# Kernel tuning notes

Measured on AMD Instinct MI355X. Metric: run time of the kernel, lower is better.

Reference implementation:

```python
import jax, jax.numpy as jnp
import numpy as np


def setup_inputs() -> dict:
    key = jax.random.key(0)
    k1, k2 = jax.random.split(key)
    N, T, D = 65536, 128, 2
    source = jax.random.normal(k1, (N, T, D), dtype=jnp.float32)
    mask = jax.random.randint(k2, (N, T, D), 0, 2).astype(jnp.float32)
    # Fixed (non-trainable) inertia-model matrices, as in the torch module.
    A = jnp.array([[0.0, 0.0, -1.0, 0.0],
                   [0.0, 0.0, 0.0, -1.0],
                   [0.0, 0.0, 0.0, 0.0],
                   [0.0, 0.0, 0.0, 0.0]], dtype=jnp.float32)
    B = jnp.array([[1.0, 0.0, 1.0, 0.0],
                   [0.0, 1.0, 0.0, 1.0]], dtype=jnp.float32)
    C = jnp.array([[0.0, 0.0],
                   [0.0, 0.0],
                   [1.0, 0.0],
                   [0.0, 1.0]], dtype=jnp.float32)
    return {"source": source, "mask": mask, "A": A, "B": B, "C": C,
            "burn_in_steps": 64}


def reference(source, mask, A, B, C, burn_in_steps):
    # use_mask=True variant of the Inertia model.
    N, T, D = source.shape
    state_dim = 4
    burn_in = int(burn_in_steps)

    src_t = jnp.swapaxes(source, 0, 1)  # [T, N, D]
    msk_t = jnp.swapaxes(mask, 0, 1)    # [T, N, D]
    ts = jnp.arange(T)

    s0 = jnp.zeros((N, state_dim), dtype=source.dtype)
    m0 = jnp.zeros((N, D), dtype=source.dtype)
    y0 = jnp.zeros((N, D), dtype=source.dtype)  # never used on first step

    def step(carry, inp):
        s, m, y = carry
        x_t, mask_t, t = inp
        in_burn = (burn_in <= 0) | (t < burn_in)  # scalar bool
        m_prev = m
        m_new = jnp.where(in_burn, mask_t, m)     # mask only advances in burn-in
        s_app = (1.0 - m_prev) * m_new            # [N, 2]
        x = jnp.where(in_burn, x_t, y)
        s_temp = s @ A + x @ B                    # [N, 4]
        s_next = jnp.concatenate(
            [s_temp[:, :2],
             s[:, 2:4] * s_app + s_temp[:, 2:4] * (1.0 - s_app)], axis=1)
        del_x = s_next @ C                        # [N, 2]
        y_new = x + del_x
        return (s_next, m_new, y_new), y_new

    _, pred = jax.lax.scan(step, (s0, m0, y0), (src_t, msk_t, ts))
    return jnp.swapaxes(pred, 0, 1)  # [N, T, D]
```

## Files before the change

### kernel.cpp

```cpp
#include <hip/hip_runtime.h>


__global__ __launch_bounds__(256) void inertia_scan(
    const float* __restrict__ src, const float* __restrict__ msk,
    float* __restrict__ out, int nseq)
{
    const int n = (blockIdx.x * 256 + threadIdx.x) >> 6;
    const int lane = threadIdx.x & 63;
    if (n >= nseq) return;
    const size_t base = (size_t)n * 128;
    const float2* __restrict__ s2 = (const float2*)src + base;
    const float2* __restrict__ m2 = (const float2*)msk + base;
    float2* __restrict__ o2 = (float2*)out + base;

    float2 sv = s2[lane];
    float2 mv = m2[lane];

    float spx = __shfl_up(sv.x, 1, 64);
    float spy = __shfl_up(sv.y, 1, 64);
    float mpx = __shfl_up(mv.x, 1, 64);
    float mpy = __shfl_up(mv.y, 1, 64);
    const bool l0 = (lane == 0);
    spx = l0 ? 0.f : spx;  spy = l0 ? 0.f : spy;
    mpx = l0 ? 0.f : mpx;  mpy = l0 ? 0.f : mpy;

    float A0 = (1.f - mpx) * mv.x;
    float A1 = (1.f - mpy) * mv.y;
    float B0 = (sv.x - spx) * (1.f - A0);
    float B1 = (sv.y - spy) * (1.f - A1);

#pragma unroll
    for (int off = 1; off < 64; off <<= 1) {
        float Ap0 = __shfl_up(A0, off, 64);
        float Bp0 = __shfl_up(B0, off, 64);
        float Ap1 = __shfl_up(A1, off, 64);
        float Bp1 = __shfl_up(B1, off, 64);
        const bool act = (lane >= off);
        Ap0 = act ? Ap0 : 1.f;  Bp0 = act ? Bp0 : 0.f;
        Ap1 = act ? Ap1 : 1.f;  Bp1 = act ? Bp1 : 0.f;
        B0 = fmaf(Bp0, A0, B0);  A0 *= Ap0;
        B1 = fmaf(Bp1, A1, B1);  A1 *= Ap1;
    }

    const float y0 = sv.x + B0;
    const float y1 = sv.y + B1;
    o2[lane] = make_float2(y0, y1);

    const float q63x = __shfl(B0, 63, 64);
    const float q63y = __shfl(B1, 63, 64);
    const float y63x = __shfl(y0, 63, 64);
    const float y63y = __shfl(y1, 63, 64);
    const float tj = (float)(lane + 1);
    o2[64 + lane] = make_float2(fmaf(tj, q63x, y63x), fmaf(tj, q63y, y63y));
}

extern "C" void kernel_launch(void* const* d_in, const int* in_sizes, int n_in,
                              void* d_out, int out_size, void* d_ws, size_t ws_size,
                              hipStream_t stream) {
    const float* src = (const float*)d_in[0];
    const float* msk = (const float*)d_in[1];
    float* out = (float*)d_out;
    const int nseq = in_sizes[0] / 256;
    const int block = 256;
    const int grid = (nseq + 3) / 4;
    inertia_scan<<<grid, block, 0, stream>>>(src, msk, out, nseq);
}
```

Baseline: 159.9 us.

## Replace shuffle-based affine scan with ballot lookup of last reset lane

Because the mask is binary, each recurrence coefficient A is either 0 or 1, and B is zero wherever A is 1. The prefix result is therefore just B at the most recent lane where A is 0. The six-step log-depth shuffle scan is replaced by one ballot per channel, a leading-zero count and a single shuffle, cutting cross-lane traffic and ALU work. This assumes mask values are exactly 0 or 1; non-binary masks would give wrong results.

```diff
diff --git a/kernel.cpp b/kernel.cpp
--- a/kernel.cpp
+++ b/kernel.cpp
@@ -24,30 +24,28 @@
     spx = l0 ? 0.f : spx;  spy = l0 ? 0.f : spy;
     mpx = l0 ? 0.f : mpx;  mpy = l0 ? 0.f : mpy;
 
-    float A0 = (1.f - mpx) * mv.x;
-    float A1 = (1.f - mpy) * mv.y;
-    float B0 = (sv.x - spx) * (1.f - A0);
-    float B1 = (sv.y - spy) * (1.f - A1);
+    const float A0 = (1.f - mpx) * mv.x;
+    const float A1 = (1.f - mpy) * mv.y;
+    const float B0 = (sv.x - spx) * (1.f - A0);
+    const float B1 = (sv.y - spy) * (1.f - A1);
 
-#pragma unroll
-    for (int off = 1; off < 64; off <<= 1) {
-        float Ap0 = __shfl_up(A0, off, 64);
-        float Bp0 = __shfl_up(B0, off, 64);
-        float Ap1 = __shfl_up(A1, off, 64);
-        float Bp1 = __shfl_up(B1, off, 64);
-        const bool act = (lane >= off);
-        Ap0 = act ? Ap0 : 1.f;  Bp0 = act ? Bp0 : 0.f;
-        Ap1 = act ? Ap1 : 1.f;  Bp1 = act ? Bp1 : 0.f;
-        B0 = fmaf(Bp0, A0, B0);  A0 *= Ap0;
-        B1 = fmaf(Bp1, A1, B1);  A1 *= Ap1;
-    }
+    const unsigned long long le = (~0ULL) >> (63 - lane);
+    const unsigned long long z0 = __ballot(A0 == 0.f) & le;
+    const unsigned long long z1 = __ballot(A1 == 0.f) & le;
 
-    const float y0 = sv.x + B0;
-    const float y1 = sv.y + B1;
+    const int r0 = z0 ? (63 - __builtin_clzll(z0)) : 0;
+    const int r1 = z1 ? (63 - __builtin_clzll(z1)) : 0;
+    const float g0 = __shfl(B0, r0, 64);
+    const float g1 = __shfl(B1, r1, 64);
+    const float q0 = z0 ? g0 : 0.f;
+    const float q1 = z1 ? g1 : 0.f;
+
+    const float y0 = sv.x + q0;
+    const float y1 = sv.y + q1;
     o2[lane] = make_float2(y0, y1);
 
-    const float q63x = __shfl(B0, 63, 64);
-    const float q63y = __shfl(B1, 63, 64);
+    const float q63x = __shfl(q0, 63, 64);
+    const float q63y = __shfl(q1, 63, 64);
     const float y63x = __shfl(y0, 63, 64);
     const float y63y = __shfl(y1, 63, 64);
     const float tj = (float)(lane + 1);
```

Measured after the change: 158.1 us. Within noise of the previous version (-1.2%).
